# Optimization experiments

Hardware: AMD Instinct MI355X
Metric: run time of the kernel (lower is better)

## Reference

```python
import jax, jax.numpy as jnp
import numpy as np

V, H, NH, FF, L = 30522, 768, 12, 3072, 2
B, S = 64, 128
EPS = 1e-12


def _ln(x, g, b):
    m = x.mean(-1, keepdims=True)
    v = jnp.var(x, axis=-1, keepdims=True)
    return (x - m) / jnp.sqrt(v + EPS) * g + b


def setup_inputs() -> dict:
    key = jax.random.key(0)
    ks = jax.random.split(key, 16)
    p = lambda k, shape: jax.random.normal(k, shape, jnp.float32) * 0.02
    return {
        "input_ids": jax.random.randint(ks[0], (B, S), 1, V).astype(jnp.int32),
        "token_type_ids": jnp.zeros((B, S), jnp.int32),
        "word_emb": p(ks[1], (V, H)),
        "pos_emb3": p(ks[2], (3, H)),
        "type_emb": p(ks[3], (2, H)),
        "emb_ln_g": jnp.ones((H,)), "emb_ln_b": jnp.zeros((H,)),
        "Wq": p(ks[4], (L, H, H)), "bq": jnp.zeros((L, H)),
        "Wk": p(ks[5], (L, H, H)), "bk": jnp.zeros((L, H)),
        "Wv": p(ks[6], (L, H, H)), "bv": jnp.zeros((L, H)),
        "Wo": p(ks[7], (L, H, H)), "bo": jnp.zeros((L, H)),
        "ln1_g": jnp.ones((L, H)), "ln1_b": jnp.zeros((L, H)),
        "W1": p(ks[8], (L, H, FF)), "b1": jnp.zeros((L, FF)),
        "W2": p(ks[9], (L, FF, H)), "b2": jnp.zeros((L, H)),
        "ln2_g": jnp.ones((L, H)), "ln2_b": jnp.zeros((L, H)),
        "Wg": p(ks[10], (H, H)), "bg": jnp.zeros((H,)),
        "pos_emb2": p(ks[11], (S, H)),
        "type_emb2": p(ks[12], (2, H)),
        "norm_g": jnp.ones((H,)), "norm_b": jnp.zeros((H,)),
    }


def _forward(input_ids, token_type_ids, word_emb, pos_emb3, type_emb,
             emb_ln_g, emb_ln_b, Wq, bq, Wk, bk, Wv, bv, Wo, bo,
             ln1_g, ln1_b, W1, b1, W2, b2, ln2_g, ln2_b,
             Wg, bg, pos_emb2, type_emb2, norm_g, norm_b):
    b, s = input_ids.shape
    # --- build trigram ids: row j = (prev, cur, next); one zero separator row per example ---
    prev = jnp.pad(input_ids, ((0, 0), (1, 0)))[:, :-1]
    nxt = jnp.pad(input_ids, ((0, 0), (0, 1)))[:, 1:]
    tri = jnp.stack([prev, input_ids, nxt], -1)                      # [B,S,3]
    tri = jnp.concatenate([tri, jnp.zeros((b, 1, 3), tri.dtype)], 1)  # [B,S+1,3]
    tri = tri.reshape(b * (s + 1), 3)                                # [N,3]
    mask = (tri > 0).astype(jnp.float32).at[:, 1].set(1.0)           # [N,3]
    bias = (1.0 - mask)[:, None, None, :] * -10000.0                 # extended attn mask

    # --- embeddings over trigram rows (token_type defaults to 0) ---
    x = word_emb[tri] + pos_emb3[None] + type_emb[0][None, None]
    x = _ln(x, emb_ln_g, emb_ln_b)

    dh = H // NH
    scale = float(1.0 / np.sqrt(dh))
    for i in range(L):  # shallow BERT layers, seq len = 3
        q = (x @ Wq[i] + bq[i]).reshape(-1, 3, NH, dh)
        k = (x @ Wk[i] + bk[i]).reshape(-1, 3, NH, dh)
        v = (x @ Wv[i] + bv[i]).reshape(-1, 3, NH, dh)
        scores = jnp.einsum('nqhd,nkhd->nhqk', q, k) * scale + bias
        a = jax.nn.softmax(scores, -1)
        c = jnp.einsum('nhqk,nkhd->nqhd', a, v).reshape(-1, 3, H)
        x = _ln(x + c @ Wo[i] + bo[i], ln1_g[i], ln1_b[i])
        f = jax.nn.gelu(x @ W1[i] + b1[i], approximate=False)
        x = _ln(x + f @ W2[i] + b2[i], ln2_g[i], ln2_b[i])

    # zero rows whose center token is padding, then sigmoid gate + mask
    center_ok = (tri[:, 1] > 0).astype(x.dtype)
    x = x * center_ok[:, None, None]
    x = x * jax.nn.sigmoid(x @ Wg + bg) * mask[..., None]

    # --- merge_ngrams: each token sums its 3 trigram appearances (vectorized shifted add) ---
    flat = x[:, 1]
    flat = flat.at[:-1].add(x[1:, 0]).at[1:].add(x[:-1, 2])
    hs = flat.reshape(b, s + 1, H)[:, :s]                            # drop separator rows

    aux = pos_emb2[None, :s] + type_emb2[token_type_ids]
    return _ln(hs + aux, norm_g, norm_b)


def reference(input_ids, token_type_ids, word_emb, pos_emb3, type_emb,
              emb_ln_g, emb_ln_b, Wq, bq, Wk, bk, Wv, bv, Wo, bo,
              ln1_g, ln1_b, W1, b1, W2, b2, ln2_g, ln2_b,
              Wg, bg, pos_emb2, type_emb2, norm_g, norm_b):
    return _forward(input_ids, token_type_ids, word_emb, pos_emb3, type_emb,
                    emb_ln_g, emb_ln_b, Wq, bq, Wk, bk, Wv, bv, Wo, bo,
                    ln1_g, ln1_b, W1, b1, W2, b2, ln2_g, ln2_b,
                    Wg, bg, pos_emb2, type_emb2, norm_g, norm_b)
```

## Files before the change

kernel.cpp:

```cpp
#include <hip/hip_runtime.h>
#include <math.h>

typedef unsigned short u16;
typedef unsigned int   u32;

#define H_    768
#define FF_   3072
#define L_    2
#define B_    64
#define S_    128
#define SP1   129
#define NROWS (B_*SP1)
#define M_    (NROWS*3)
#define MPAD  24832
#define MT_   (MPAD/128)

typedef __attribute__((ext_vector_type(8))) short s16x8;
typedef __attribute__((ext_vector_type(4))) float f32x4;

__device__ __forceinline__ float bf2f(u16 u){ union{u32 i; float f;} c; c.i=((u32)u)<<16; return c.f; }
__device__ __forceinline__ u16 f2bf(float x){ union{float f; u32 i;} c; c.f=x; u32 r=c.i+0x7fffu+((c.i>>16)&1u); return (u16)(r>>16); }

__device__ __forceinline__ void bf4u(uint2 u, float* v){
  v[0]=bf2f((u16)(u.x&0xffffu)); v[1]=bf2f((u16)(u.x>>16));
  v[2]=bf2f((u16)(u.y&0xffffu)); v[3]=bf2f((u16)(u.y>>16));
}
__device__ __forceinline__ uint2 fpack4(const float* v){
  u32 lo=(u32)f2bf(v[0]) | ((u32)f2bf(v[1])<<16);
  u32 hi=(u32)f2bf(v[2]) | ((u32)f2bf(v[3])<<16);
  return make_uint2(lo,hi);
}
__device__ __forceinline__ float wredf(float v){
  #pragma unroll
  for (int o=32;o;o>>=1) v += __shfl_xor(v,o,64);
  return v;
}

typedef const __attribute__((address_space(1))) void* gas1_t;
typedef __attribute__((address_space(3))) void*       las3_t;
__device__ __forceinline__ void gload16(const void* g, void* l){
  __builtin_amdgcn_global_load_lds((gas1_t)g, (las3_t)l, 16, 0, 0);
}

struct TP9 { const float* s[9]; u16* d[9]; };

__global__ __launch_bounds__(256) void tconv_k(TP9 P, int Rr, int Cc){
  __shared__ u16 tle[32][33];
  const float* src = P.s[blockIdx.z];
  u16* dst = P.d[blockIdx.z];
  int c0 = blockIdx.x*32, r0 = blockIdx.y*32;
  int tx = threadIdx.x&31, ty = threadIdx.x>>5;
  #pragma unroll
  for (int i=0;i<32;i+=8) tle[ty+i][tx] = f2bf(src[(size_t)(r0+ty+i)*Cc + (c0+tx)]);
  __syncthreads();
  #pragma unroll
  for (int i=0;i<32;i+=8) dst[(size_t)(c0+ty+i)*Rr + (r0+tx)] = tle[tx][ty+i];
}

__global__ __launch_bounds__(256) void embed_k(const int* __restrict__ ids, const float* __restrict__ wemb,
    const float* __restrict__ pe3, const float* __restrict__ te, const float* __restrict__ gg,
    const float* __restrict__ bb, u16* __restrict__ x)
{
  int m = (int)((blockIdx.x*256u + threadIdx.x)>>6);
  int lane = threadIdx.x&63;
  size_t base = (size_t)m*H_;
  if (m >= M_){
    #pragma unroll
    for (int k3=0;k3<3;k3++){ int col=lane*4+k3*256; *(uint2*)&x[base+col]=make_uint2(0u,0u); }
    return;
  }
  int n = m/3, j = m - n*3;
  int bi = n/SP1, sp = n - bi*SP1;
  int id = 0;
  if (sp < S_){
    int s2 = sp + j - 1;
    if (s2 >= 0 && s2 < S_) id = ids[bi*S_ + s2];
  }
  const float* wr = wemb + (size_t)id*H_;
  const float* pr = pe3 + j*H_;
  float vals[12]; float s=0.f, sq=0.f;
  #pragma unroll
  for (int k3=0;k3<3;k3++){
    int col = lane*4 + k3*256;
    float4 wv = *(const float4*)(wr+col);
    float4 pv = *(const float4*)(pr+col);
    float4 tv = *(const float4*)(te+col);
    float a0=wv.x+pv.x+tv.x, a1=wv.y+pv.y+tv.y, a2=wv.z+pv.z+tv.z, a3=wv.w+pv.w+tv.w;
    vals[k3*4+0]=a0; vals[k3*4+1]=a1; vals[k3*4+2]=a2; vals[k3*4+3]=a3;
    s += a0+a1+a2+a3; sq += a0*a0+a1*a1+a2*a2+a3*a3;
  }
  s = wredf(s); sq = wredf(sq);
  float mean = s*(1.f/H_);
  float var  = sq*(1.f/H_) - mean*mean;
  float rstd = rsqrtf(fmaxf(var,0.f)+1e-12f);
  #pragma unroll
  for (int k3=0;k3<3;k3++){
    int col = lane*4 + k3*256;
    float o[4];
    #pragma unroll
    for (int t=0;t<4;t++) o[t] = (vals[k3*4+t]-mean)*rstd*gg[col+t] + bb[col+t];
    *(uint2*)&x[base+col] = fpack4(o);
  }
}

__global__ __launch_bounds__(256) void ln_k(const u16* __restrict__ in, const float* __restrict__ gg,
    const float* __restrict__ bb, u16* __restrict__ out)
{
  int row = (int)((blockIdx.x*256u + threadIdx.x)>>6);
  int lane = threadIdx.x&63;
  size_t base = (size_t)row*H_;
  float vals[12]; float s=0.f, sq=0.f;
  #pragma unroll
  for (int k3=0;k3<3;k3++){
    int col = lane*4+k3*256;
    float v[4]; bf4u(*(const uint2*)&in[base+col], v);
    #pragma unroll
    for (int t=0;t<4;t++){ vals[k3*4+t]=v[t]; s+=v[t]; sq+=v[t]*v[t]; }
  }
  s=wredf(s); sq=wredf(sq);
  float mean=s*(1.f/H_);
  float var=sq*(1.f/H_)-mean*mean;
  float rstd=rsqrtf(fmaxf(var,0.f)+1e-12f);
  #pragma unroll
  for (int k3=0;k3<3;k3++){
    int col=lane*4+k3*256;
    float o[4];
    #pragma unroll
    for (int t=0;t<4;t++) o[t]=(vals[k3*4+t]-mean)*rstd*gg[col+t]+bb[col+t];
    *(uint2*)&out[base+col]=fpack4(o);
  }
}

__global__ __launch_bounds__(256) void attn_k(const u16* Q, const u16* Kt, const u16* Vt, u16* O)
{
  int gw = (int)((blockIdx.x*256u + threadIdx.x)>>6);
  int lane = threadIdx.x&63;
  int n = gw/12, h = gw - n*12;
  int sp = n % SP1;
  size_t base = (size_t)n*3*H_ + h*64 + lane;
  float q[3],k[3],v[3];
  #pragma unroll
  for (int j=0;j<3;j++){
    q[j]=bf2f(Q[base+(size_t)j*H_]);
    k[j]=bf2f(Kt[base+(size_t)j*H_]);
    v[j]=bf2f(Vt[base+(size_t)j*H_]);
  }
  float sc[9];
  #pragma unroll
  for (int a=0;a<3;a++)
    #pragma unroll
    for (int b=0;b<3;b++) sc[a*3+b]=q[a]*k[b];
  #pragma unroll
  for (int o=32;o;o>>=1){
    #pragma unroll
    for (int t=0;t<9;t++) sc[t]+=__shfl_xor(sc[t],o,64);
  }
  float b0 = (sp>=1 && sp<S_) ? 0.f : -1e4f;
  float b2 = (sp<S_-1) ? 0.f : -1e4f;
  #pragma unroll
  for (int a=0;a<3;a++){
    float s0=sc[a*3+0]*0.125f+b0;
    float s1=sc[a*3+1]*0.125f;
    float s2=sc[a*3+2]*0.125f+b2;
    float mx=fmaxf(s0,fmaxf(s1,s2));
    float e0=expf(s0-mx), e1=expf(s1-mx), e2=expf(s2-mx);
    float cv=(e0*v[0]+e1*v[1]+e2*v[2])/(e0+e1+e2);
    O[base+(size_t)a*H_]=f2bf(cv);
  }
}

template<int EPI>
__global__ __launch_bounds__(256) void gemm_k(const u16* __restrict__ A, int lda,
    const u16* __restrict__ Bt, const float* __restrict__ bias,
    const u16* __restrict__ R, int ldr, u16* __restrict__ C, int ldc, int K)
{
  __shared__ u16 As[128*32];
  __shared__ u16 Bs[128*32];
  const int tid = threadIdx.x;
  const int wave = tid>>6, lane = tid&63;
  const int wm = (wave>>1)*64, wn = (wave&1)*64;
  const int fr = lane&15, kg = lane>>4;
  f32x4 acc[4][4];
  #pragma unroll
  for (int i=0;i<4;i++)
    #pragma unroll
    for (int j=0;j<4;j++) acc[i][j] = (f32x4){0.f,0.f,0.f,0.f};

  const int ldab = lda*2, ldbb = K*2;
  const char* Ab = (const char*)(A + (size_t)blockIdx.x*128*lda);
  const char* Bb = (const char*)(Bt + (size_t)blockIdx.y*128*K);
  char* AsB = (char*)As; char* BsB = (char*)Bs;
  const int s0r = tid>>2,       s0c = (tid&3)*16;
  const int s1r = s0r + 64,     s1c = s0c;
  const int wofs = wave*1024;

  for (int kt=0; kt<K; kt+=32){
    const int kb = kt*2;
    gload16(Ab + (size_t)s0r*ldab + kb + s0c, AsB + wofs);
    gload16(Ab + (size_t)s1r*ldab + kb + s1c, AsB + 4096 + wofs);
    gload16(Bb + (size_t)s0r*ldbb + kb + s0c, BsB + wofs);
    gload16(Bb + (size_t)s1r*ldbb + kb + s1c, BsB + 4096 + wofs);
    __syncthreads();
    s16x8 af[4], bfr[4];
    #pragma unroll
    for (int i=0;i<4;i++) af[i]  = *(const s16x8*)(AsB + (size_t)((wm+i*16+fr)*64 + kg*16));
    #pragma unroll
    for (int j=0;j<4;j++) bfr[j] = *(const s16x8*)(BsB + (size_t)((wn+j*16+fr)*64 + kg*16));
    #pragma unroll
    for (int i=0;i<4;i++)
      #pragma unroll
      for (int j=0;j<4;j++)
        acc[i][j] = __builtin_amdgcn_mfma_f32_16x16x32_bf16(af[i], bfr[j], acc[i][j], 0,0,0);
    __syncthreads();
  }

  const int gr0 = (int)blockIdx.x*128 + wm + (lane>>4)*4;
  const int gc0 = (int)blockIdx.y*128 + wn + fr;
  #pragma unroll
  for (int j=0;j<4;j++){
    const int col = gc0 + j*16;
    const float bc = bias[col];
    #pragma unroll
    for (int i=0;i<4;i++){
      #pragma unroll
      for (int r=0;r<4;r++){
        const int row = gr0 + i*16 + r;
        float v = acc[i][j][r] + bc;
        if (EPI==1) v += bf2f(R[(size_t)row*ldr + col]);
        if (EPI==2) v = 0.5f*v*(1.f+erff(v*0.70710678118654752f));
        if (EPI==3){
          float xv = bf2f(R[(size_t)row*ldr + col]);
          int nn = row/3, j3 = row - nn*3;
          int sp = nn % SP1;
          float mk = (j3==1) ? 1.f : ((j3==0) ? (((sp>=1)&&(sp<S_))?1.f:0.f) : ((sp<S_-1)?1.f:0.f));
          v = xv * (1.f/(1.f+expf(-v))) * mk;
        }
        C[(size_t)row*ldc + col] = f2bf(v);
      }
    }
  }
}

__global__ __launch_bounds__(256) void final_k(const u16* __restrict__ G, const int* __restrict__ tt,
    const float* __restrict__ pe2, const float* __restrict__ te2, const float* __restrict__ gg,
    const float* __restrict__ bb, float* __restrict__ out)
{
  int r = (int)((blockIdx.x*256u+threadIdx.x)>>6);
  int lane = threadIdx.x&63;
  int bi = r>>7, sp = r&127;
  int n = bi*SP1+sp;
  int t = tt[r];
  size_t g1 = ((size_t)n*3+1)*H_;
  size_t g0 = ((size_t)(n+1)*3+0)*H_;
  size_t g2 = (n>0) ? ((size_t)(n-1)*3+2)*H_ : 0;
  const float* p2 = pe2 + (size_t)sp*H_;
  const float* t2 = te2 + (size_t)t*H_;
  float vals[12]; float s=0.f, sq=0.f;
  #pragma unroll
  for (int k3=0;k3<3;k3++){
    int col=lane*4+k3*256;
    float a[4], b[4], c[4]={0.f,0.f,0.f,0.f};
    bf4u(*(const uint2*)&G[g1+col], a);
    bf4u(*(const uint2*)&G[g0+col], b);
    if (n>0) bf4u(*(const uint2*)&G[g2+col], c);
    #pragma unroll
    for (int q=0;q<4;q++){
      float v = a[q]+b[q]+c[q] + p2[col+q] + t2[col+q];
      vals[k3*4+q]=v; s+=v; sq+=v*v;
    }
  }
  s=wredf(s); sq=wredf(sq);
  float mean=s*(1.f/H_), var=sq*(1.f/H_)-mean*mean;
  float rstd=rsqrtf(fmaxf(var,0.f)+1e-12f);
  #pragma unroll
  for (int k3=0;k3<3;k3++){
    int col=lane*4+k3*256;
    float4 o;
    o.x=(vals[k3*4+0]-mean)*rstd*gg[col+0]+bb[col+0];
    o.y=(vals[k3*4+1]-mean)*rstd*gg[col+1]+bb[col+1];
    o.z=(vals[k3*4+2]-mean)*rstd*gg[col+2]+bb[col+2];
    o.w=(vals[k3*4+3]-mean)*rstd*gg[col+3]+bb[col+3];
    *(float4*)&out[(size_t)r*H_+col]=o;
  }
}

extern "C" void kernel_launch(void* const* d_in, const int* in_sizes, int n_in,
                              void* d_out, int out_size, void* d_ws, size_t ws_size,
                              hipStream_t stream)
{
  (void)in_sizes; (void)n_in; (void)out_size;
  const int*   ids  = (const int*)d_in[0];
  const int*   tt   = (const int*)d_in[1];
  const float* wemb = (const float*)d_in[2];
  const float* pe3  = (const float*)d_in[3];
  const float* te   = (const float*)d_in[4];
  const float* elg  = (const float*)d_in[5];
  const float* elb  = (const float*)d_in[6];
  const float* Wq   = (const float*)d_in[7];
  const float* bq   = (const float*)d_in[8];
  const float* Wk   = (const float*)d_in[9];
  const float* bk   = (const float*)d_in[10];
  const float* Wv   = (const float*)d_in[11];
  const float* bv   = (const float*)d_in[12];
  const float* Wo   = (const float*)d_in[13];
  const float* bo   = (const float*)d_in[14];
  const float* l1g  = (const float*)d_in[15];
  const float* l1b  = (const float*)d_in[16];
  const float* W1   = (const float*)d_in[17];
  const float* b1   = (const float*)d_in[18];
  const float* W2   = (const float*)d_in[19];
  const float* b2   = (const float*)d_in[20];
  const float* l2g  = (const float*)d_in[21];
  const float* l2b  = (const float*)d_in[22];
  const float* Wg   = (const float*)d_in[23];
  const float* bg   = (const float*)d_in[24];
  const float* pe2  = (const float*)d_in[25];
  const float* te2  = (const float*)d_in[26];
  const float* ng   = (const float*)d_in[27];
  const float* nb   = (const float*)d_in[28];

  char* p = (char*)d_ws;
  auto alloc = [&](size_t bytes)->char*{
    char* r = p; p += (bytes + 255) & ~((size_t)255); return r;
  };
  const size_t HH = (size_t)H_*H_;
  u16* wtq = (u16*)alloc((size_t)L_*HH*2);
  u16* wtk = (u16*)alloc((size_t)L_*HH*2);
  u16* wtv = (u16*)alloc((size_t)L_*HH*2);
  u16* wto = (u16*)alloc((size_t)L_*HH*2);
  u16* wt1 = (u16*)alloc((size_t)L_*H_*FF_*2);
  u16* wt2 = (u16*)alloc((size_t)L_*H_*FF_*2);
  u16* wtg = (u16*)alloc(HH*2);
  u16* xb  = (u16*)alloc((size_t)MPAD*H_*2);
  u16* qb  = (u16*)alloc((size_t)MPAD*H_*2);
  u16* kbf = (u16*)alloc((size_t)MPAD*H_*2);
  u16* vbf = (u16*)alloc((size_t)MPAD*H_*2);
  size_t used = (size_t)(p - (char*)d_ws);
  size_t avail = ws_size > used ? ws_size - used : 0;
  long long mrows = (long long)(avail / ((size_t)FF_*2));
  int strip = (int)((mrows/128)*128);
  if (strip > MPAD) strip = MPAD;
  if (strip < 128) strip = 128;
  u16* fbf = (u16*)alloc((size_t)strip*FF_*2);

  {
    TP9 P;
    P.s[0]=Wq;     P.d[0]=wtq;
    P.s[1]=Wq+HH;  P.d[1]=wtq+HH;
    P.s[2]=Wk;     P.d[2]=wtk;
    P.s[3]=Wk+HH;  P.d[3]=wtk+HH;
    P.s[4]=Wv;     P.d[4]=wtv;
    P.s[5]=Wv+HH;  P.d[5]=wtv+HH;
    P.s[6]=Wo;     P.d[6]=wto;
    P.s[7]=Wo+HH;  P.d[7]=wto+HH;
    P.s[8]=Wg;     P.d[8]=wtg;
    tconv_k<<<dim3(H_/32, H_/32, 9), 256, 0, stream>>>(P, H_, H_);
  }
  {
    TP9 P; for (int i=0;i<9;i++){P.s[i]=Wq;P.d[i]=wtq;}
    P.s[0]=W1;                 P.d[0]=wt1;
    P.s[1]=W1+(size_t)H_*FF_;  P.d[1]=wt1+(size_t)H_*FF_;
    tconv_k<<<dim3(FF_/32, H_/32, 2), 256, 0, stream>>>(P, H_, FF_);
  }
  {
    TP9 P; for (int i=0;i<9;i++){P.s[i]=Wq;P.d[i]=wtq;}
    P.s[0]=W2;                 P.d[0]=wt2;
    P.s[1]=W2+(size_t)H_*FF_;  P.d[1]=wt2+(size_t)H_*FF_;
    tconv_k<<<dim3(H_/32, FF_/32, 2), 256, 0, stream>>>(P, FF_, H_);
  }

  embed_k<<<MPAD/4, 256, 0, stream>>>(ids, wemb, pe3, te, elg, elb, xb);

  for (int i=0;i<L_;i++){
    const u16* wq_i = wtq + (size_t)i*HH;
    const u16* wk_i = wtk + (size_t)i*HH;
    const u16* wv_i = wtv + (size_t)i*HH;
    const u16* wo_i = wto + (size_t)i*HH;
    const u16* w1_i = wt1 + (size_t)i*H_*FF_;
    const u16* w2_i = wt2 + (size_t)i*H_*FF_;
    gemm_k<0><<<dim3(MT_,6),256,0,stream>>>(xb, H_, wq_i, bq+(size_t)i*H_, (const u16*)0, 0, qb,  H_, H_);
    gemm_k<0><<<dim3(MT_,6),256,0,stream>>>(xb, H_, wk_i, bk+(size_t)i*H_, (const u16*)0, 0, kbf, H_, H_);
    gemm_k<0><<<dim3(MT_,6),256,0,stream>>>(xb, H_, wv_i, bv+(size_t)i*H_, (const u16*)0, 0, vbf, H_, H_);
    attn_k<<<(NROWS*12)/4, 256, 0, stream>>>(qb, kbf, vbf, qb);
    gemm_k<1><<<dim3(MT_,6),256,0,stream>>>(qb, H_, wo_i, bo+(size_t)i*H_, xb, H_, kbf, H_, H_);
    ln_k<<<M_/4,256,0,stream>>>(kbf, l1g+(size_t)i*H_, l1b+(size_t)i*H_, xb);
    for (int s0=0; s0<MPAD; s0+=strip){
      int rows = MPAD - s0; if (rows > strip) rows = strip;
      gemm_k<2><<<dim3(rows/128,FF_/128),256,0,stream>>>(xb+(size_t)s0*H_, H_, w1_i, b1+(size_t)i*FF_,
                                                         (const u16*)0, 0, fbf, FF_, H_);
      gemm_k<1><<<dim3(rows/128,6),256,0,stream>>>(fbf, FF_, w2_i, b2+(size_t)i*H_,
                                                   xb+(size_t)s0*H_, H_, kbf+(size_t)s0*H_, H_, FF_);
    }
    ln_k<<<M_/4,256,0,stream>>>(kbf, l2g+(size_t)i*H_, l2b+(size_t)i*H_, xb);
  }
  gemm_k<3><<<dim3(MT_,6),256,0,stream>>>(xb, H_, wtg, bg, xb, H_, kbf, H_, H_);
  final_k<<<(B_*S_)/4, 256, 0, stream>>>(kbf, tt, pe2, te2, ng, nb, (float*)d_out);
}
```

Measured before the change: 2.063 ms.

## Fuse QKV GEMMs, double-buffer GEMM LDS, add XCD-aware tile swizzle

Concatenates the Q, K and V weights and biases so one GEMM with N=2304 replaces three launches, and attention reads and writes the packed QKV buffer in place. The GEMM kernel gains double-buffered LDS staging so the next K-tile loads while MFMAs run, s_setprio around the MFMA block, a 1D grid remapped so consecutive tiles land on the same XCD, and launch bounds of 4 blocks per CU. These target launch overhead, load latency and L2 locality, at the cost of twice the LDS per block and a wider activation stride into the output projection.

Result: faster. 1.739 ms (-15.7%).

```diff
diff --git a/kernel.cpp b/kernel.cpp
--- a/kernel.cpp
+++ b/kernel.cpp
@@ -14,6 +14,7 @@
 #define M_    (NROWS*3)
 #define MPAD  24832
 #define MT_   (MPAD/128)
+#define QKV_N 2304
 
 typedef __attribute__((ext_vector_type(8))) short s16x8;
 typedef __attribute__((ext_vector_type(4))) float f32x4;
@@ -55,6 +56,14 @@
   __syncthreads();
   #pragma unroll
   for (int i=0;i<32;i+=8) dst[(size_t)(c0+ty+i)*Rr + (r0+tx)] = tle[tx][ty+i];
+}
+
+__global__ __launch_bounds__(256) void bcat_k(const float* bq, const float* bk, const float* bv, float* dst){
+  int i = (int)(blockIdx.x*256u + threadIdx.x);
+  if (i >= L_*QKV_N) return;
+  int l = i/QKV_N, c = i - l*QKV_N;
+  float v = (c<H_) ? bq[l*H_+c] : (c<2*H_) ? bk[l*H_+c-H_] : bv[l*H_+c-2*H_];
+  dst[i] = v;
 }
 
 __global__ __launch_bounds__(256) void embed_k(const int* __restrict__ ids, const float* __restrict__ wemb,
@@ -131,19 +140,19 @@
   }
 }
 
-__global__ __launch_bounds__(256) void attn_k(const u16* Q, const u16* Kt, const u16* Vt, u16* O)
+__global__ __launch_bounds__(256) void attn_k(u16* QKV)
 {
   int gw = (int)((blockIdx.x*256u + threadIdx.x)>>6);
   int lane = threadIdx.x&63;
   int n = gw/12, h = gw - n*12;
   int sp = n % SP1;
-  size_t base = (size_t)n*3*H_ + h*64 + lane;
+  size_t base = (size_t)n*3*QKV_N + h*64 + lane;
   float q[3],k[3],v[3];
   #pragma unroll
   for (int j=0;j<3;j++){
-    q[j]=bf2f(Q[base+(size_t)j*H_]);
-    k[j]=bf2f(Kt[base+(size_t)j*H_]);
-    v[j]=bf2f(Vt[base+(size_t)j*H_]);
+    q[j]=bf2f(QKV[base+(size_t)j*QKV_N]);
+    k[j]=bf2f(QKV[base+(size_t)j*QKV_N + H_]);
+    v[j]=bf2f(QKV[base+(size_t)j*QKV_N + 2*H_]);
   }
   float sc[9];
   #pragma unroll
@@ -165,21 +174,28 @@
     float mx=fmaxf(s0,fmaxf(s1,s2));
     float e0=expf(s0-mx), e1=expf(s1-mx), e2=expf(s2-mx);
     float cv=(e0*v[0]+e1*v[1]+e2*v[2])/(e0+e1+e2);
-    O[base+(size_t)a*H_]=f2bf(cv);
+    QKV[base+(size_t)a*QKV_N]=f2bf(cv);
   }
 }
 
 template<int EPI>
-__global__ __launch_bounds__(256) void gemm_k(const u16* __restrict__ A, int lda,
+__global__ __launch_bounds__(256,4) void gemm_k(const u16* __restrict__ A, int lda,
     const u16* __restrict__ Bt, const float* __restrict__ bias,
-    const u16* __restrict__ R, int ldr, u16* __restrict__ C, int ldc, int K)
-{
-  __shared__ u16 As[128*32];
-  __shared__ u16 Bs[128*32];
+    const u16* __restrict__ R, int ldr, u16* __restrict__ C, int ldc, int K, int NT)
+{
+  __shared__ u16 As[2][4096];
+  __shared__ u16 Bs[2][4096];
   const int tid = threadIdx.x;
   const int wave = tid>>6, lane = tid&63;
   const int wm = (wave>>1)*64, wn = (wave&1)*64;
   const int fr = lane&15, kg = lane>>4;
+
+  const int nwg = (int)gridDim.x;
+  const int qq = nwg>>3, rr = nwg&7;
+  const int xcd = (int)blockIdx.x&7, idx = (int)blockIdx.x>>3;
+  const int swz = (xcd<rr ? xcd*(qq+1) : rr*(qq+1) + (xcd-rr)*qq) + idx;
+  const int bx = swz/NT, by = swz - bx*NT;
+
   f32x4 acc[4][4];
   #pragma unroll
   for (int i=0;i<4;i++)
@@ -187,35 +203,48 @@
     for (int j=0;j<4;j++) acc[i][j] = (f32x4){0.f,0.f,0.f,0.f};
 
   const int ldab = lda*2, ldbb = K*2;
-  const char* Ab = (const char*)(A + (size_t)blockIdx.x*128*lda);
-  const char* Bb = (const char*)(Bt + (size_t)blockIdx.y*128*K);
-  char* AsB = (char*)As; char* BsB = (char*)Bs;
-  const int s0r = tid>>2,       s0c = (tid&3)*16;
-  const int s1r = s0r + 64,     s1c = s0c;
+  const char* Ab = (const char*)(A + (size_t)bx*128*lda);
+  const char* Bb = (const char*)(Bt + (size_t)by*128*K);
+  const int s0r = tid>>2, s0c = (tid&3)*16;
+  const int s1r = s0r + 64;
   const int wofs = wave*1024;
 
-  for (int kt=0; kt<K; kt+=32){
-    const int kb = kt*2;
-    gload16(Ab + (size_t)s0r*ldab + kb + s0c, AsB + wofs);
-    gload16(Ab + (size_t)s1r*ldab + kb + s1c, AsB + 4096 + wofs);
-    gload16(Bb + (size_t)s0r*ldbb + kb + s0c, BsB + wofs);
-    gload16(Bb + (size_t)s1r*ldbb + kb + s1c, BsB + 4096 + wofs);
-    __syncthreads();
+  auto stage = [&](int buf, int kt){
+    const int kb = kt*64;
+    char* ad = (char*)(&As[buf][0]) + wofs;
+    char* bd = (char*)(&Bs[buf][0]) + wofs;
+    gload16(Ab + (size_t)s0r*ldab + kb + s0c, ad);
+    gload16(Ab + (size_t)s1r*ldab + kb + s0c, ad + 4096);
+    gload16(Bb + (size_t)s0r*ldbb + kb + s0c, bd);
+    gload16(Bb + (size_t)s1r*ldbb + kb + s0c, bd + 4096);
+  };
+
+  const int nt = K>>5;
+  stage(0, 0);
+  __syncthreads();
+  int cur = 0;
+  for (int t=0; t<nt; ++t){
+    if (t+1 < nt) stage(cur^1, t+1);
+    const char* AsB = (const char*)(&As[cur][0]);
+    const char* BsB = (const char*)(&Bs[cur][0]);
     s16x8 af[4], bfr[4];
     #pragma unroll
-    for (int i=0;i<4;i++) af[i]  = *(const s16x8*)(AsB + (size_t)((wm+i*16+fr)*64 + kg*16));
-    #pragma unroll
-    for (int j=0;j<4;j++) bfr[j] = *(const s16x8*)(BsB + (size_t)((wn+j*16+fr)*64 + kg*16));
+    for (int i=0;i<4;i++) af[i]  = *(const s16x8*)(AsB + ((wm+i*16+fr)<<6) + (kg<<4));
+    #pragma unroll
+    for (int j=0;j<4;j++) bfr[j] = *(const s16x8*)(BsB + ((wn+j*16+fr)<<6) + (kg<<4));
+    __builtin_amdgcn_s_setprio(1);
     #pragma unroll
     for (int i=0;i<4;i++)
       #pragma unroll
       for (int j=0;j<4;j++)
         acc[i][j] = __builtin_amdgcn_mfma_f32_16x16x32_bf16(af[i], bfr[j], acc[i][j], 0,0,0);
+    __builtin_amdgcn_s_setprio(0);
     __syncthreads();
-  }
-
-  const int gr0 = (int)blockIdx.x*128 + wm + (lane>>4)*4;
-  const int gc0 = (int)blockIdx.y*128 + wn + fr;
+    cur ^= 1;
+  }
+
+  const int gr0 = bx*128 + wm + (lane>>4)*4;
+  const int gc0 = by*128 + wn + fr;
   #pragma unroll
   for (int j=0;j<4;j++){
     const int col = gc0 + j*16;
@@ -324,17 +353,15 @@
     char* r = p; p += (bytes + 255) & ~((size_t)255); return r;
   };
   const size_t HH = (size_t)H_*H_;
-  u16* wtq = (u16*)alloc((size_t)L_*HH*2);
-  u16* wtk = (u16*)alloc((size_t)L_*HH*2);
-  u16* wtv = (u16*)alloc((size_t)L_*HH*2);
-  u16* wto = (u16*)alloc((size_t)L_*HH*2);
-  u16* wt1 = (u16*)alloc((size_t)L_*H_*FF_*2);
-  u16* wt2 = (u16*)alloc((size_t)L_*H_*FF_*2);
-  u16* wtg = (u16*)alloc(HH*2);
-  u16* xb  = (u16*)alloc((size_t)MPAD*H_*2);
-  u16* qb  = (u16*)alloc((size_t)MPAD*H_*2);
-  u16* kbf = (u16*)alloc((size_t)MPAD*H_*2);
-  u16* vbf = (u16*)alloc((size_t)MPAD*H_*2);
+  u16*  wqkv = (u16*)alloc((size_t)L_*3*HH*2);
+  u16*  wto  = (u16*)alloc((size_t)L_*HH*2);
+  u16*  wt1  = (u16*)alloc((size_t)L_*H_*FF_*2);
+  u16*  wt2  = (u16*)alloc((size_t)L_*H_*FF_*2);
+  u16*  wtg  = (u16*)alloc(HH*2);
+  float* bqkv= (float*)alloc((size_t)L_*QKV_N*4);
+  u16*  xb   = (u16*)alloc((size_t)MPAD*H_*2);
+  u16*  qkv  = (u16*)alloc((size_t)MPAD*QKV_N*2);
+  u16*  kbf  = (u16*)alloc((size_t)MPAD*H_*2);
   size_t used = (size_t)(p - (char*)d_ws);
   size_t avail = ws_size > used ? ws_size - used : 0;
   long long mrows = (long long)(avail / ((size_t)FF_*2));
@@ -345,54 +372,52 @@
 
   {
     TP9 P;
-    P.s[0]=Wq;     P.d[0]=wtq;
-    P.s[1]=Wq+HH;  P.d[1]=wtq+HH;
-    P.s[2]=Wk;     P.d[2]=wtk;
-    P.s[3]=Wk+HH;  P.d[3]=wtk+HH;
-    P.s[4]=Wv;     P.d[4]=wtv;
-    P.s[5]=Wv+HH;  P.d[5]=wtv+HH;
+    P.s[0]=Wq;     P.d[0]=wqkv;
+    P.s[1]=Wk;     P.d[1]=wqkv+HH;
+    P.s[2]=Wv;     P.d[2]=wqkv+2*HH;
+    P.s[3]=Wq+HH;  P.d[3]=wqkv+3*HH;
+    P.s[4]=Wk+HH;  P.d[4]=wqkv+4*HH;
+    P.s[5]=Wv+HH;  P.d[5]=wqkv+5*HH;
     P.s[6]=Wo;     P.d[6]=wto;
     P.s[7]=Wo+HH;  P.d[7]=wto+HH;
     P.s[8]=Wg;     P.d[8]=wtg;
     tconv_k<<<dim3(H_/32, H_/32, 9), 256, 0, stream>>>(P, H_, H_);
   }
   {
-    TP9 P; for (int i=0;i<9;i++){P.s[i]=Wq;P.d[i]=wtq;}
+    TP9 P; for (int i=0;i<9;i++){P.s[i]=Wq;P.d[i]=wtg;}
     P.s[0]=W1;                 P.d[0]=wt1;
     P.s[1]=W1+(size_t)H_*FF_;  P.d[1]=wt1+(size_t)H_*FF_;
     tconv_k<<<dim3(FF_/32, H_/32, 2), 256, 0, stream>>>(P, H_, FF_);
   }
   {
-    TP9 P; for (int i=0;i<9;i++){P.s[i]=Wq;P.d[i]=wtq;}
+    TP9 P; for (int i=0;i<9;i++){P.s[i]=Wq;P.d[i]=wtg;}
     P.s[0]=W2;                 P.d[0]=wt2;
     P.s[1]=W2+(size_t)H_*FF_;  P.d[1]=wt2+(size_t)H_*FF_;
     tconv_k<<<dim3(H_/32, FF_/32, 2), 256, 0, stream>>>(P, FF_, H_);
   }
+  bcat_k<<<(L_*QKV_N+255)/256, 256, 0, stream>>>(bq, bk, bv, bqkv);
 
   embed_k<<<MPAD/4, 256, 0, stream>>>(ids, wemb, pe3, te, elg, elb, xb);
 
   for (int i=0;i<L_;i++){
-    const u16* wq_i = wtq + (size_t)i*HH;
-    const u16* wk_i = wtk + (size_t)i*HH;
-    const u16* wv_i = wtv + (size_t)i*HH;
-    const u16* wo_i = wto + (size_t)i*HH;
-    const u16* w1_i = wt1 + (size_t)i*H_*FF_;
-    const u16* w2_i = wt2 + (size_t)i*H_*FF_;
-    gemm_k<0><<<dim3(MT_,6),256,0,stream>>>(xb, H_, wq_i, bq+(size_t)i*H_, (const u16*)0, 0, qb,  H_, H_);
-    gemm_k<0><<<dim3(MT_,6),256,0,stream>>>(xb, H_, wk_i, bk+(size_t)i*H_, (const u16*)0, 0, kbf, H_, H_);
-    gemm_k<0><<<dim3(MT_,6),256,0,stream>>>(xb, H_, wv_i, bv+(size_t)i*H_, (const u16*)0, 0, vbf, H_, H_);
-    attn_k<<<(NROWS*12)/4, 256, 0, stream>>>(qb, kbf, vbf, qb);
-    gemm_k<1><<<dim3(MT_,6),256,0,stream>>>(qb, H_, wo_i, bo+(size_t)i*H_, xb, H_, kbf, H_, H_);
+    const u16* wqkv_i = wqkv + (size_t)i*3*HH;
+    const u16* wo_i   = wto  + (size_t)i*HH;
+    const u16* w1_i   = wt1  + (size_t)i*H_*FF_;
+    const u16* w2_i   = wt2  + (size_t)i*H_*FF_;
+    gemm_k<0><<<MT_*18,256,0,stream>>>(xb, H_, wqkv_i, bqkv+(size_t)i*QKV_N,
+                                       (const u16*)0, 0, qkv, QKV_N, H_, 18);
+    attn_k<<<(NROWS*12)/4, 256, 0, stream>>>(qkv);
+    gemm_k<1><<<MT_*6,256,0,stream>>>(qkv, QKV_N, wo_i, bo+(size_t)i*H_, xb, H_, kbf, H_, H_, 6);
     ln_k<<<M_/4,256,0,stream>>>(kbf, l1g+(size_t)i*H_, l1b+(size_t)i*H_, xb);
     for (int s0=0; s0<MPAD; s0+=strip){
       int rows = MPAD - s0; if (rows > strip) rows = strip;
-      gemm_k<2><<<dim3(rows/128,FF_/128),256,0,stream>>>(xb+(size_t)s0*H_, H_, w1_i, b1+(size_t)i*FF_,
-                                                         (const u16*)0, 0, fbf, FF_, H_);
-      gemm_k<1><<<dim3(rows/128,6),256,0,stream>>>(fbf, FF_, w2_i, b2+(size_t)i*H_,
-                                                   xb+(size_t)s0*H_, H_, kbf+(size_t)s0*H_, H_, FF_);
+      gemm_k<2><<<(rows/128)*24,256,0,stream>>>(xb+(size_t)s0*H_, H_, w1_i, b1+(size_t)i*FF_,
+                                                (const u16*)0, 0, fbf, FF_, H_, 24);
+      gemm_k<1><<<(rows/128)*6,256,0,stream>>>(fbf, FF_, w2_i, b2+(size_t)i*H_,
+                                               xb+(size_t)s0*H_, H_, kbf+(size_t)s0*H_, H_, FF_, 6);
     }
     ln_k<<<M_/4,256,0,stream>>>(kbf, l2g+(size_t)i*H_, l2b+(size_t)i*H_, xb);
   }
-  gemm_k<3><<<dim3(MT_,6),256,0,stream>>>(xb, H_, wtg, bg, xb, H_, kbf, H_, H_);
+  gemm_k<3><<<MT_*6,256,0,stream>>>(xb, H_, wtg, bg, xb, H_, kbf, H_, H_, 6);
   final_k<<<(B_*S_)/4, 256, 0, stream>>>(kbf, tt, pe2, te2, ng, nb, (float*)d_out);
 }
```
